# Kernel optimization log

Hardware: AMD Instinct MI355X
Metric: run time of the kernel (lower is better)

## Reference

```python
import jax, jax.numpy as jnp
import numpy as np

DIM = 256
HEADS = 8
H = 56
W = 56
WS = 7          # window size
SHIFT = 3       # cyclic shift
MLP_HIDDEN = 4 * DIM
HEAD_DIM = DIM // HEADS
SCALE = HEAD_DIM ** -0.5
N = WS * WS     # tokens per window
EPS = 1e-5


def _rel_pos_index():
    coords = np.stack(np.meshgrid(np.arange(WS), np.arange(WS), indexing='ij'))  # [2,ws,ws]
    cf = coords.reshape(2, -1)                       # [2, N]
    rel = cf[:, :, None] - cf[:, None, :]            # [2, N, N]
    rel = rel.transpose(1, 2, 0).copy()              # [N, N, 2]
    rel[:, :, 0] += WS - 1
    rel[:, :, 1] += WS - 1
    rel[:, :, 1] *= 2 * WS - 1
    return rel.sum(-1)                               # [N, N]

REL_IDX = jnp.asarray(_rel_pos_index())


def _attn_mask():
    # shifted-window attention mask, computed once (static)
    img = np.zeros((H, W))
    cnt = 0
    slices = (slice(0, -WS), slice(-WS, -SHIFT), slice(-SHIFT, None))
    for hs in slices:
        for ws in slices:
            img[hs, ws] = cnt
            cnt += 1
    mw = img.reshape(H // WS, WS, W // WS, WS).transpose(0, 2, 1, 3).reshape(-1, N)  # [nW, N]
    am = mw[:, None, :] - mw[:, :, None]
    return jnp.asarray(np.where(am != 0, -100.0, 0.0).astype(np.float32))  # [nW, N, N]

ATTN_MASK = _attn_mask()


def _layernorm(y, g, b):
    mu = y.mean(-1, keepdims=True)
    var = ((y - mu) ** 2).mean(-1, keepdims=True)
    return (y - mu) * jax.lax.rsqrt(var + EPS) * g + b


def setup_inputs() -> dict:
    key = jax.random.key(0)
    ks = jax.random.split(key, 10)
    B = 32
    x = jax.random.normal(ks[0], (B, H * W, DIM), dtype=jnp.float32)
    qkv_w = jax.random.normal(ks[1], (DIM, 3 * DIM), dtype=jnp.float32) * 0.02
    qkv_b = jnp.zeros((3 * DIM,), dtype=jnp.float32)
    proj_w = jax.random.normal(ks[2], (DIM, DIM), dtype=jnp.float32) * 0.02
    proj_b = jnp.zeros((DIM,), dtype=jnp.float32)
    bias_table = jax.random.normal(ks[3], ((2 * WS - 1) * (2 * WS - 1), HEADS), dtype=jnp.float32) * 0.02
    norm1_g = jnp.ones((DIM,), dtype=jnp.float32)
    norm1_b = jnp.zeros((DIM,), dtype=jnp.float32)
    norm2_g = jnp.ones((DIM,), dtype=jnp.float32)
    norm2_b = jnp.zeros((DIM,), dtype=jnp.float32)
    mlp_w1 = jax.random.normal(ks[4], (DIM, MLP_HIDDEN), dtype=jnp.float32) * 0.02
    mlp_b1 = jnp.zeros((MLP_HIDDEN,), dtype=jnp.float32)
    mlp_w2 = jax.random.normal(ks[5], (MLP_HIDDEN, DIM), dtype=jnp.float32) * 0.02
    mlp_b2 = jnp.zeros((DIM,), dtype=jnp.float32)
    return dict(x=x, norm1_g=norm1_g, norm1_b=norm1_b, qkv_w=qkv_w, qkv_b=qkv_b,
                proj_w=proj_w, proj_b=proj_b, bias_table=bias_table,
                norm2_g=norm2_g, norm2_b=norm2_b,
                mlp_w1=mlp_w1, mlp_b1=mlp_b1, mlp_w2=mlp_w2, mlp_b2=mlp_b2)


def reference(x, norm1_g, norm1_b, qkv_w, qkv_b, proj_w, proj_b, bias_table,
              norm2_g, norm2_b, mlp_w1, mlp_b1, mlp_w2, mlp_b2):
    B, M, C = x.shape
    shortcut = x
    y = _layernorm(x, norm1_g, norm1_b).reshape(B, H, W, C)
    # cyclic shift
    y = jnp.roll(y, (-SHIFT, -SHIFT), axis=(1, 2))
    # window partition: [B,H,W,C] -> [B*nW, N, C]
    win = y.reshape(B, H // WS, WS, W // WS, WS, C).transpose(0, 1, 3, 2, 4, 5).reshape(-1, N, C)
    Bw = win.shape[0]
    qkv = (win @ qkv_w + qkv_b).reshape(Bw, N, 3, HEADS, HEAD_DIM).transpose(2, 0, 3, 1, 4)
    q, k, v = qkv[0], qkv[1], qkv[2]               # each [Bw, heads, N, hd]
    attn = jnp.einsum('bhnd,bhmd->bhnm', q, k) * SCALE
    bias = bias_table[REL_IDX].transpose(2, 0, 1)  # [heads, N, N]
    attn = attn + bias[None]
    nW = ATTN_MASK.shape[0]
    attn = attn.reshape(B, nW, HEADS, N, N) + ATTN_MASK[None, :, None]
    attn = jax.nn.softmax(attn.reshape(Bw, HEADS, N, N), axis=-1)
    out = jnp.einsum('bhnm,bhmd->bhnd', attn, v).transpose(0, 2, 1, 3).reshape(Bw, N, C)
    out = out @ proj_w + proj_b
    # window reverse and un-shift
    out = out.reshape(B, H // WS, W // WS, WS, WS, C).transpose(0, 1, 3, 2, 4, 5).reshape(B, H, W, C)
    out = jnp.roll(out, (SHIFT, SHIFT), axis=(1, 2)).reshape(B, M, C)
    x = shortcut + out
    h = _layernorm(x, norm2_g, norm2_b)
    h = jax.nn.gelu(h @ mlp_w1 + mlp_b1) @ mlp_w2 + mlp_b2
    return x + h
```

## Files before the change

### kernel.cpp

```cpp
#include <hip/hip_runtime.h>
#include <hip/hip_bf16.h>
#include <math.h>

typedef __bf16 bf16_t;
typedef __attribute__((ext_vector_type(8))) __bf16 bf16x8;
typedef __attribute__((ext_vector_type(4))) __bf16 bf16x4;
typedef __attribute__((ext_vector_type(4))) float f32x4;

#define T_TOK 100352
#define DIMC 256
#define HEADS 8
#define HD 32
#define NTOK 49
#define SHIFT3 3
#define HH 56
#define SCALE_QK 0.17677669529663687f

__device__ __forceinline__ int xrow_of(int rr) {
    int wi = rr / 49; int t = rr - wi * 49;
    int b = wi >> 6; int w64 = wi & 63;
    int wh = w64 >> 3, ww = w64 & 7;
    int i = t / 7, j = t - i * 7;
    int hy = wh * 7 + i, wy = ww * 7 + j;
    int hx = hy + SHIFT3; if (hx >= HH) hx -= HH;
    int wx = wy + SHIFT3; if (wx >= HH) wx -= HH;
    return b * (HH * HH) + hx * HH + wx;
}

__global__ __launch_bounds__(256) void transpose_cast(const float* __restrict__ W,
                                                      bf16_t* __restrict__ WT,
                                                      int K, int Nc) {
    int t = blockIdx.x * 256 + threadIdx.x;
    int k = t / Nc, c = t - k * Nc;
    WT[(size_t)c * K + k] = (bf16_t)W[t];
}

template <int MAP>
__global__ __launch_bounds__(256) void ln_kernel(const float* __restrict__ x,
                                                 const float* __restrict__ g,
                                                 const float* __restrict__ bsh,
                                                 bf16_t* __restrict__ out) {
    int wv = threadIdx.x >> 6, l = threadIdx.x & 63;
    int r = blockIdx.x * 4 + wv;
    int xr = MAP ? xrow_of(r) : r;
    float4 v = ((const float4*)(x + (size_t)xr * DIMC))[l];
    float s = v.x + v.y + v.z + v.w;
    float sq = v.x * v.x + v.y * v.y + v.z * v.z + v.w * v.w;
    #pragma unroll
    for (int off = 32; off; off >>= 1) {
        s += __shfl_down(s, off);
        sq += __shfl_down(sq, off);
    }
    s = __shfl(s, 0); sq = __shfl(sq, 0);
    float mean = s * (1.f / 256.f);
    float var = sq * (1.f / 256.f) - mean * mean;
    float rstd = rsqrtf(var + 1e-5f);
    float4 gv = ((const float4*)g)[l];
    float4 bv = ((const float4*)bsh)[l];
    bf16x4 o;
    o[0] = (bf16_t)((v.x - mean) * rstd * gv.x + bv.x);
    o[1] = (bf16_t)((v.y - mean) * rstd * gv.y + bv.y);
    o[2] = (bf16_t)((v.z - mean) * rstd * gv.z + bv.z);
    o[3] = (bf16_t)((v.w - mean) * rstd * gv.w + bv.w);
    *(bf16x4*)(out + (size_t)r * DIMC + l * 4) = o;
}

template <int EPI, int KT>
__global__ __launch_bounds__(256) void gemm128(const bf16_t* __restrict__ A,
                                               const bf16_t* __restrict__ BT,
                                               const float* __restrict__ bias,
                                               int Nc,
                                               bf16_t* __restrict__ outb,
                                               float* __restrict__ outf,
                                               const float* __restrict__ resid) {
    constexpr int NS = KT / 64;
    __shared__ bf16_t As[2][128 * 64];
    __shared__ bf16_t Bs[2][128 * 64];
    int tid = threadIdx.x;
    int wv = tid >> 6, l = tid & 63;
    int wr = wv >> 1, wc = wv & 1;
    int nTilesN = Nc >> 7;
    int qn = gridDim.x >> 3;
    int lb = (blockIdx.x & 7) * qn + (blockIdx.x >> 3);
    int bm = lb / nTilesN, bn = lb - bm * nTilesN;
    size_t row0 = (size_t)bm * 128;
    int col0 = bn * 128;

    const char* Abase = (const char*)(A + row0 * KT);
    const char* Bbase = (const char*)(BT + (size_t)col0 * KT);
    const size_t ldb = (size_t)KT * 2;

    auto STAGE = [&](int buf, int kk) {
        #pragma unroll
        for (int it = 0; it < 4; ++it) {
            int ci = tid + it * 256;
            int row = ci >> 3, ch = ci & 7;
            int sc = ch ^ (row & 7);
            __builtin_amdgcn_global_load_lds(
                (const __attribute__((address_space(1))) void*)(Abase + (size_t)row * ldb + (size_t)kk * 2 + sc * 16),
                (__attribute__((address_space(3))) void*)((char*)As[buf] + ci * 16), 16, 0, 0);
            __builtin_amdgcn_global_load_lds(
                (const __attribute__((address_space(1))) void*)(Bbase + (size_t)row * ldb + (size_t)kk * 2 + sc * 16),
                (__attribute__((address_space(3))) void*)((char*)Bs[buf] + ci * 16), 16, 0, 0);
        }
    };

    f32x4 acc[4][4] = {};
    const int lr = l & 15, g4 = l >> 4;

    STAGE(0, 0);
    if (NS > 1) STAGE(1, 64);

    #pragma unroll
    for (int s = 0; s < NS; ++s) {
        if (s + 1 < NS) { asm volatile("s_waitcnt vmcnt(8)" ::: "memory"); }
        else            { asm volatile("s_waitcnt vmcnt(0)" ::: "memory"); }
        __builtin_amdgcn_s_barrier();
        __builtin_amdgcn_sched_barrier(0);
        int buf = s & 1;
        #pragma unroll
        for (int ks = 0; ks < 2; ++ks) {
            bf16x8 a[4], b[4];
            #pragma unroll
            for (int mt = 0; mt < 4; ++mt) {
                int rr = wr * 64 + mt * 16 + lr;
                int c = (ks * 4 + g4) ^ (rr & 7);
                a[mt] = *(const bf16x8*)((char*)As[buf] + rr * 128 + c * 16);
            }
            #pragma unroll
            for (int nt = 0; nt < 4; ++nt) {
                int rc = wc * 64 + nt * 16 + lr;
                int c = (ks * 4 + g4) ^ (rc & 7);
                b[nt] = *(const bf16x8*)((char*)Bs[buf] + rc * 128 + c * 16);
            }
            __builtin_amdgcn_s_setprio(1);
            #pragma unroll
            for (int mt = 0; mt < 4; ++mt)
                #pragma unroll
                for (int nt = 0; nt < 4; ++nt)
                    acc[mt][nt] = __builtin_amdgcn_mfma_f32_16x16x32_bf16(a[mt], b[nt], acc[mt][nt], 0, 0, 0);
            __builtin_amdgcn_s_setprio(0);
        }
        __builtin_amdgcn_s_barrier();
        __builtin_amdgcn_sched_barrier(0);
        if (s + 2 < NS) STAGE(buf, (s + 2) * 64);
    }

    #pragma unroll
    for (int m = 0; m < 4; ++m) {
        #pragma unroll
        for (int i = 0; i < 4; ++i) {
            int rr = (int)row0 + wr * 64 + m * 16 + g4 * 4 + i;
            size_t orow = (EPI == 3) ? (size_t)xrow_of(rr) * DIMC : (size_t)rr * Nc;
            #pragma unroll
            for (int n = 0; n < 4; ++n) {
                int cc = col0 + wc * 64 + n * 16 + lr;
                float v = acc[m][n][i] + bias[cc];
                if (EPI == 0) {
                    outb[(size_t)rr * Nc + cc] = (bf16_t)v;
                } else if (EPI == 1) {
                    float t3 = v + 0.044715f * v * v * v;
                    float e = __expf(-1.5957691216057308f * t3);
                    float gl = v * __builtin_amdgcn_rcpf(1.f + e);
                    outb[(size_t)rr * Nc + cc] = (bf16_t)gl;
                } else if (EPI == 2) {
                    size_t o = (size_t)rr * Nc + cc;
                    outf[o] = v + resid[o];
                } else {
                    size_t o = orow + cc;
                    outf[o] = v + resid[o];
                }
            }
        }
    }
}

__global__ __launch_bounds__(256) void attn_mfma(const bf16_t* __restrict__ qkv,
                                                 const float* __restrict__ bt,
                                                 bf16_t* __restrict__ out) {
    __shared__ __align__(16) char lds[4][12800];
    int wv = threadIdx.x >> 6, l = threadIdx.x & 63;
    int head = ((blockIdx.x & 1) << 2) | wv;
    int wi = blockIdx.x >> 1;
    char* W = lds[wv];
    bf16_t* Vt = (bf16_t*)(W + 8192);
    size_t rowbase = (size_t)wi * NTOK;
    const bf16_t* src = qkv + rowbase * 768 + head * HD;

    int w64 = wi & 63;
    int wh = w64 >> 3, ww = w64 & 7;
    bool lastH = (wh == 7), lastW = (ww == 7);
    bool masked = lastH || lastW;

    #pragma unroll
    for (int it = 0; it < 4; ++it) {
        int t = l + it * 64;
        int r = t >> 2, g = t & 3;
        if (r < NTOK) {
            bf16x8 qv = *(const bf16x8*)(src + (size_t)r * 768 + g * 8);
            bf16x8 kv = *(const bf16x8*)(src + (size_t)r * 768 + 256 + g * 8);
            int sa = (r * 64 + g * 16) ^ ((r & 7) << 4);
            *(bf16x8*)(W + sa) = qv;
            *(bf16x8*)(W + 4096 + sa) = kv;
        }
    }
    #pragma unroll
    for (int it = 0; it < 4; ++it) {
        int t = l + it * 64;
        int m = t >> 2, dc = t & 3;
        if (m < NTOK) {
            bf16x8 vv = *(const bf16x8*)(src + (size_t)m * 768 + 512 + dc * 8);
            #pragma unroll
            for (int j = 0; j < 8; ++j) Vt[(dc * 8 + j) * 72 + m] = vv[j];
        } else {
            #pragma unroll
            for (int j = 0; j < 8; ++j) Vt[(dc * 8 + j) * 72 + m] = (bf16_t)0.f;
        }
    }

    int lr = l & 15, g4 = l >> 4;

    bf16x8 a[4], b[4];
    #pragma unroll
    for (int mt = 0; mt < 4; ++mt) {
        int r = mt * 16 + lr;
        int sa = (r * 64 + g4 * 16) ^ ((r & 7) << 4);
        a[mt] = *(const bf16x8*)(W + sa);
        b[mt] = *(const bf16x8*)(W + 4096 + sa);
    }
    f32x4 z = {0.f, 0.f, 0.f, 0.f};
    f32x4 S[4][4];
    #pragma unroll
    for (int mt = 0; mt < 4; ++mt)
        #pragma unroll
        for (int nt = 0; nt < 4; ++nt)
            S[mt][nt] = __builtin_amdgcn_mfma_f32_16x16x32_bf16(a[mt], b[nt], z, 0, 0, 0);

    int i2[4], j2[4], reg2[4];
    #pragma unroll
    for (int nt = 0; nt < 4; ++nt) {
        int cm = nt * 16 + lr;
        i2[nt] = (cm * 147) >> 10;
        j2[nt] = cm - i2[nt] * 7;
        int rh = lastH ? ((i2[nt] < 4) ? 1 : 2) : 0;
        int rw = lastW ? ((j2[nt] < 4) ? 1 : 2) : 0;
        reg2[nt] = rh * 3 + rw;
    }

    #pragma unroll
    for (int mt = 0; mt < 4; ++mt) {
        #pragma unroll
        for (int i = 0; i < 4; ++i) {
            int rn = mt * 16 + g4 * 4 + i;
            bool rowok = rn < NTOK;
            int i1 = (rn * 147) >> 10, j1 = rn - i1 * 7;
            int rh1 = lastH ? ((i1 < 4) ? 1 : 2) : 0;
            int rw1 = lastW ? ((j1 < 4) ? 1 : 2) : 0;
            int reg1 = rh1 * 3 + rw1;
            float sv[4];
            #pragma unroll
            for (int nt = 0; nt < 4; ++nt) {
                int cm = nt * 16 + lr;
                float sc;
                if (rowok && cm < NTOK) {
                    sc = S[mt][nt][i] * SCALE_QK;
                    sc += bt[((i1 - i2[nt] + 6) + 13 * (j1 - j2[nt] + 6)) * 8 + head];
                    if (masked && (reg1 != reg2[nt])) sc -= 100.f;
                } else {
                    sc = -1e30f;
                }
                sv[nt] = sc;
            }
            float mx = fmaxf(fmaxf(sv[0], sv[1]), fmaxf(sv[2], sv[3]));
            mx = fmaxf(mx, __shfl_xor(mx, 1));
            mx = fmaxf(mx, __shfl_xor(mx, 2));
            mx = fmaxf(mx, __shfl_xor(mx, 4));
            mx = fmaxf(mx, __shfl_xor(mx, 8));
            float e[4];
            float sum = 0.f;
            #pragma unroll
            for (int nt = 0; nt < 4; ++nt) { e[nt] = __expf(sv[nt] - mx); sum += e[nt]; }
            sum += __shfl_xor(sum, 1);
            sum += __shfl_xor(sum, 2);
            sum += __shfl_xor(sum, 4);
            sum += __shfl_xor(sum, 8);
            float inv = 1.f / sum;
            #pragma unroll
            for (int nt = 0; nt < 4; ++nt) {
                int cm = nt * 16 + lr;
                int pa = (rn * 128 + cm * 2) ^ ((rn & 7) << 4);
                *(bf16_t*)(W + pa) = (bf16_t)(e[nt] * inv);
            }
        }
    }

    f32x4 o[4][2] = {};
    #pragma unroll
    for (int ks = 0; ks < 2; ++ks) {
        bf16x8 pa[4], vb[2];
        #pragma unroll
        for (int mt = 0; mt < 4; ++mt) {
            int r = mt * 16 + lr;
            int ad = (r * 128 + ks * 64 + g4 * 16) ^ ((r & 7) << 4);
            pa[mt] = *(const bf16x8*)(W + ad);
        }
        #pragma unroll
        for (int dt = 0; dt < 2; ++dt) {
            int d = dt * 16 + lr;
            vb[dt] = *(const bf16x8*)((char*)Vt + d * 144 + ks * 64 + g4 * 16);
        }
        #pragma unroll
        for (int mt = 0; mt < 4; ++mt)
            #pragma unroll
            for (int dt = 0; dt < 2; ++dt)
                o[mt][dt] = __builtin_amdgcn_mfma_f32_16x16x32_bf16(pa[mt], vb[dt], o[mt][dt], 0, 0, 0);
    }

    #pragma unroll
    for (int mt = 0; mt < 4; ++mt) {
        #pragma unroll
        for (int i = 0; i < 4; ++i) {
            int n = mt * 16 + g4 * 4 + i;
            if (n < NTOK) {
                #pragma unroll
                for (int dt = 0; dt < 2; ++dt) {
                    out[(rowbase + n) * DIMC + head * HD + dt * 16 + lr] = (bf16_t)o[mt][dt][i];
                }
            }
        }
    }
}

extern "C" void kernel_launch(void* const* d_in, const int* in_sizes, int n_in,
                              void* d_out, int out_size, void* d_ws, size_t ws_size,
                              hipStream_t stream) {
    const float* x      = (const float*)d_in[0];
    const float* n1g    = (const float*)d_in[1];
    const float* n1b    = (const float*)d_in[2];
    const float* qkv_w  = (const float*)d_in[3];
    const float* qkv_b  = (const float*)d_in[4];
    const float* proj_w = (const float*)d_in[5];
    const float* proj_b = (const float*)d_in[6];
    const float* btab   = (const float*)d_in[7];
    const float* n2g    = (const float*)d_in[8];
    const float* n2b    = (const float*)d_in[9];
    const float* w1     = (const float*)d_in[10];
    const float* b1     = (const float*)d_in[11];
    const float* w2     = (const float*)d_in[12];
    const float* b2     = (const float*)d_in[13];

    char* ws = (char*)d_ws;
    bf16_t* win      = (bf16_t*)(ws);
    bf16_t* qkvbuf   = (bf16_t*)(ws + (size_t)T_TOK * 256 * 2);
    bf16_t* mlp1_buf = (bf16_t*)(ws);
    bf16_t* h2       = (bf16_t*)(ws + (size_t)T_TOK * 2048);
    char* wtp        = ws + (size_t)T_TOK * 2048 + (size_t)T_TOK * 512;
    bf16_t* wt_qkv   = (bf16_t*)wtp;
    bf16_t* wt_proj  = wt_qkv + 768 * 256;
    bf16_t* wt_mlp1  = wt_proj + 256 * 256;
    bf16_t* wt_mlp2  = wt_mlp1 + 1024 * 256;
    float* xmid      = (float*)d_out;

    transpose_cast<<<768, 256, 0, stream>>>(qkv_w, wt_qkv, 256, 768);
    transpose_cast<<<256, 256, 0, stream>>>(proj_w, wt_proj, 256, 256);
    transpose_cast<<<1024, 256, 0, stream>>>(w1, wt_mlp1, 256, 1024);
    transpose_cast<<<1024, 256, 0, stream>>>(w2, wt_mlp2, 1024, 256);

    ln_kernel<1><<<T_TOK / 4, 256, 0, stream>>>(x, n1g, n1b, win);
    gemm128<0, 256><<<(T_TOK / 128) * (768 / 128), 256, 0, stream>>>(win, wt_qkv, qkv_b, 768,
                                                                     qkvbuf, nullptr, nullptr);
    attn_mfma<<<2048 * 2, 256, 0, stream>>>(qkvbuf, btab, win);
    gemm128<3, 256><<<(T_TOK / 128) * (256 / 128), 256, 0, stream>>>(win, wt_proj, proj_b, 256,
                                                                     nullptr, xmid, x);
    ln_kernel<0><<<T_TOK / 4, 256, 0, stream>>>(xmid, n2g, n2b, h2);
    gemm128<1, 256><<<(T_TOK / 128) * (1024 / 128), 256, 0, stream>>>(h2, wt_mlp1, b1, 1024,
                                                                      mlp1_buf, nullptr, nullptr);
    gemm128<2, 1024><<<(T_TOK / 128) * (256 / 128), 256, 0, stream>>>(mlp1_buf, wt_mlp2, b2, 256,
                                                                      nullptr, xmid, xmid);
}
```

Measured before the change: 547.0 us.

## Fuse projection GEMM with residual and LayerNorm2; shrink GEMM K-tile to 32

Adds a proj_ln kernel that computes the attention output projection over 64-row by 256-column tiles. In the same kernel it adds bias and the residual, scatters rows back to the unshifted token order, and applies LayerNorm2. It writes both xmid and the bf16 normalized h2, which removes the separate LayerNorm launch and its extra pass over the fp32 activations. Separately, the generic gemm128 K-step drops from 64 to 32 with a one-stage-ahead prefetch and 4-chunk swizzle. That lowers LDS use but doubles the barriers per K.

After: 617.3 us. 12.8% more time.

```diff
diff --git a/kernel.cpp b/kernel.cpp
--- a/kernel.cpp
+++ b/kernel.cpp
@@ -35,14 +35,13 @@
     WT[(size_t)c * K + k] = (bf16_t)W[t];
 }
 
-template <int MAP>
 __global__ __launch_bounds__(256) void ln_kernel(const float* __restrict__ x,
                                                  const float* __restrict__ g,
                                                  const float* __restrict__ bsh,
                                                  bf16_t* __restrict__ out) {
     int wv = threadIdx.x >> 6, l = threadIdx.x & 63;
     int r = blockIdx.x * 4 + wv;
-    int xr = MAP ? xrow_of(r) : r;
+    int xr = xrow_of(r);
     float4 v = ((const float4*)(x + (size_t)xr * DIMC))[l];
     float s = v.x + v.y + v.z + v.w;
     float sq = v.x * v.x + v.y * v.y + v.z * v.z + v.w * v.w;
@@ -73,9 +72,9 @@
                                                bf16_t* __restrict__ outb,
                                                float* __restrict__ outf,
                                                const float* __restrict__ resid) {
-    constexpr int NS = KT / 64;
-    __shared__ bf16_t As[2][128 * 64];
-    __shared__ bf16_t Bs[2][128 * 64];
+    constexpr int NS = KT / 32;
+    __shared__ bf16_t As[2][128 * 32];
+    __shared__ bf16_t Bs[2][128 * 32];
     int tid = threadIdx.x;
     int wv = tid >> 6, l = tid & 63;
     int wr = wv >> 1, wc = wv & 1;
@@ -92,10 +91,10 @@
 
     auto STAGE = [&](int buf, int kk) {
         #pragma unroll
-        for (int it = 0; it < 4; ++it) {
+        for (int it = 0; it < 2; ++it) {
             int ci = tid + it * 256;
-            int row = ci >> 3, ch = ci & 7;
-            int sc = ch ^ (row & 7);
+            int row = ci >> 2, ch = ci & 3;
+            int sc = ch ^ (row & 3);
             __builtin_amdgcn_global_load_lds(
                 (const __attribute__((address_space(1))) void*)(Abase + (size_t)row * ldb + (size_t)kk * 2 + sc * 16),
                 (__attribute__((address_space(3))) void*)((char*)As[buf] + ci * 16), 16, 0, 0);
@@ -109,41 +108,39 @@
     const int lr = l & 15, g4 = l >> 4;
 
     STAGE(0, 0);
-    if (NS > 1) STAGE(1, 64);
-
-    #pragma unroll
+
     for (int s = 0; s < NS; ++s) {
-        if (s + 1 < NS) { asm volatile("s_waitcnt vmcnt(8)" ::: "memory"); }
-        else            { asm volatile("s_waitcnt vmcnt(0)" ::: "memory"); }
+        int buf = s & 1;
+        if (s + 1 < NS) {
+            STAGE(buf ^ 1, (s + 1) * 32);
+            asm volatile("s_waitcnt vmcnt(4)" ::: "memory");
+        } else {
+            asm volatile("s_waitcnt vmcnt(0)" ::: "memory");
+        }
         __builtin_amdgcn_s_barrier();
         __builtin_amdgcn_sched_barrier(0);
-        int buf = s & 1;
-        #pragma unroll
-        for (int ks = 0; ks < 2; ++ks) {
-            bf16x8 a[4], b[4];
-            #pragma unroll
-            for (int mt = 0; mt < 4; ++mt) {
-                int rr = wr * 64 + mt * 16 + lr;
-                int c = (ks * 4 + g4) ^ (rr & 7);
-                a[mt] = *(const bf16x8*)((char*)As[buf] + rr * 128 + c * 16);
-            }
-            #pragma unroll
-            for (int nt = 0; nt < 4; ++nt) {
-                int rc = wc * 64 + nt * 16 + lr;
-                int c = (ks * 4 + g4) ^ (rc & 7);
-                b[nt] = *(const bf16x8*)((char*)Bs[buf] + rc * 128 + c * 16);
-            }
-            __builtin_amdgcn_s_setprio(1);
-            #pragma unroll
-            for (int mt = 0; mt < 4; ++mt)
-                #pragma unroll
-                for (int nt = 0; nt < 4; ++nt)
-                    acc[mt][nt] = __builtin_amdgcn_mfma_f32_16x16x32_bf16(a[mt], b[nt], acc[mt][nt], 0, 0, 0);
-            __builtin_amdgcn_s_setprio(0);
-        }
+        bf16x8 a[4], b[4];
+        #pragma unroll
+        for (int mt = 0; mt < 4; ++mt) {
+            int rr = wr * 64 + mt * 16 + lr;
+            int c = g4 ^ (rr & 3);
+            a[mt] = *(const bf16x8*)((char*)As[buf] + rr * 64 + c * 16);
+        }
+        #pragma unroll
+        for (int nt = 0; nt < 4; ++nt) {
+            int rc = wc * 64 + nt * 16 + lr;
+            int c = g4 ^ (rc & 3);
+            b[nt] = *(const bf16x8*)((char*)Bs[buf] + rc * 64 + c * 16);
+        }
+        __builtin_amdgcn_s_setprio(1);
+        #pragma unroll
+        for (int mt = 0; mt < 4; ++mt)
+            #pragma unroll
+            for (int nt = 0; nt < 4; ++nt)
+                acc[mt][nt] = __builtin_amdgcn_mfma_f32_16x16x32_bf16(a[mt], b[nt], acc[mt][nt], 0, 0, 0);
+        __builtin_amdgcn_s_setprio(0);
+        __builtin_amdgcn_sched_barrier(0);
         __builtin_amdgcn_s_barrier();
-        __builtin_amdgcn_sched_barrier(0);
-        if (s + 2 < NS) STAGE(buf, (s + 2) * 64);
     }
 
     #pragma unroll
@@ -151,7 +148,6 @@
         #pragma unroll
         for (int i = 0; i < 4; ++i) {
             int rr = (int)row0 + wr * 64 + m * 16 + g4 * 4 + i;
-            size_t orow = (EPI == 3) ? (size_t)xrow_of(rr) * DIMC : (size_t)rr * Nc;
             #pragma unroll
             for (int n = 0; n < 4; ++n) {
                 int cc = col0 + wc * 64 + n * 16 + lr;
@@ -163,14 +159,128 @@
                     float e = __expf(-1.5957691216057308f * t3);
                     float gl = v * __builtin_amdgcn_rcpf(1.f + e);
                     outb[(size_t)rr * Nc + cc] = (bf16_t)gl;
-                } else if (EPI == 2) {
+                } else {
                     size_t o = (size_t)rr * Nc + cc;
-                    outf[o] = v + resid[o];
-                } else {
-                    size_t o = orow + cc;
                     outf[o] = v + resid[o];
                 }
             }
+        }
+    }
+}
+
+__global__ __launch_bounds__(256) void proj_ln(const bf16_t* __restrict__ A,
+                                               const bf16_t* __restrict__ BT,
+                                               const float* __restrict__ bias,
+                                               const float* __restrict__ x,
+                                               const float* __restrict__ g2,
+                                               const float* __restrict__ b2,
+                                               float* __restrict__ xmid,
+                                               bf16_t* __restrict__ h2) {
+    constexpr int NS = 8;
+    __shared__ bf16_t As[2][64 * 32];
+    __shared__ bf16_t Bs[2][256 * 32];
+    int tid = threadIdx.x;
+    int wv = tid >> 6, l = tid & 63;
+    int lr = l & 15, g4 = l >> 4;
+    int qn = gridDim.x >> 3;
+    int lb = (blockIdx.x & 7) * qn + (blockIdx.x >> 3);
+    size_t row0 = (size_t)lb * 64;
+
+    const char* Abase = (const char*)(A + row0 * 256);
+    const char* Bbase = (const char*)BT;
+
+    auto STAGE = [&](int buf, int kk) {
+        {
+            int ci = tid;
+            int row = ci >> 2, ch = ci & 3;
+            int sc = ch ^ (row & 3);
+            __builtin_amdgcn_global_load_lds(
+                (const __attribute__((address_space(1))) void*)(Abase + (size_t)row * 512 + (size_t)kk * 2 + sc * 16),
+                (__attribute__((address_space(3))) void*)((char*)As[buf] + ci * 16), 16, 0, 0);
+        }
+        #pragma unroll
+        for (int it = 0; it < 4; ++it) {
+            int ci = tid + it * 256;
+            int row = ci >> 2, ch = ci & 3;
+            int sc = ch ^ (row & 3);
+            __builtin_amdgcn_global_load_lds(
+                (const __attribute__((address_space(1))) void*)(Bbase + (size_t)row * 512 + (size_t)kk * 2 + sc * 16),
+                (__attribute__((address_space(3))) void*)((char*)Bs[buf] + ci * 16), 16, 0, 0);
+        }
+    };
+
+    f32x4 acc[16] = {};
+
+    STAGE(0, 0);
+
+    for (int s = 0; s < NS; ++s) {
+        int buf = s & 1;
+        if (s + 1 < NS) {
+            STAGE(buf ^ 1, (s + 1) * 32);
+            asm volatile("s_waitcnt vmcnt(5)" ::: "memory");
+        } else {
+            asm volatile("s_waitcnt vmcnt(0)" ::: "memory");
+        }
+        __builtin_amdgcn_s_barrier();
+        __builtin_amdgcn_sched_barrier(0);
+        bf16x8 a;
+        {
+            int rr = wv * 16 + lr;
+            int c = g4 ^ (rr & 3);
+            a = *(const bf16x8*)((char*)As[buf] + rr * 64 + c * 16);
+        }
+        bf16x8 b[16];
+        #pragma unroll
+        for (int nt = 0; nt < 16; ++nt) {
+            int rc = nt * 16 + lr;
+            int c = g4 ^ (rc & 3);
+            b[nt] = *(const bf16x8*)((char*)Bs[buf] + rc * 64 + c * 16);
+        }
+        __builtin_amdgcn_s_setprio(1);
+        #pragma unroll
+        for (int nt = 0; nt < 16; ++nt)
+            acc[nt] = __builtin_amdgcn_mfma_f32_16x16x32_bf16(a, b[nt], acc[nt], 0, 0, 0);
+        __builtin_amdgcn_s_setprio(0);
+        __builtin_amdgcn_sched_barrier(0);
+        __builtin_amdgcn_s_barrier();
+    }
+
+    int xr[4];
+    #pragma unroll
+    for (int i = 0; i < 4; ++i) xr[i] = xrow_of((int)row0 + wv * 16 + g4 * 4 + i);
+
+    float psum[4] = {0.f, 0.f, 0.f, 0.f}, psq[4] = {0.f, 0.f, 0.f, 0.f};
+    #pragma unroll
+    for (int n = 0; n < 16; ++n) {
+        int cc = n * 16 + lr;
+        float bv = bias[cc];
+        #pragma unroll
+        for (int i = 0; i < 4; ++i) {
+            float v = acc[n][i] + bv + x[(size_t)xr[i] * 256 + cc];
+            psum[i] += v; psq[i] += v * v;
+        }
+    }
+    float mean[4], rstd[4];
+    #pragma unroll
+    for (int i = 0; i < 4; ++i) {
+        float s = psum[i], q = psq[i];
+        s += __shfl_xor(s, 1); q += __shfl_xor(q, 1);
+        s += __shfl_xor(s, 2); q += __shfl_xor(q, 2);
+        s += __shfl_xor(s, 4); q += __shfl_xor(q, 4);
+        s += __shfl_xor(s, 8); q += __shfl_xor(q, 8);
+        mean[i] = s * (1.f / 256.f);
+        rstd[i] = rsqrtf(q * (1.f / 256.f) - mean[i] * mean[i] + 1e-5f);
+    }
+    #pragma unroll
+    for (int n = 0; n < 16; ++n) {
+        int cc = n * 16 + lr;
+        float bv = bias[cc], gv = g2[cc], b2v = b2[cc];
+        #pragma unroll
+        for (int i = 0; i < 4; ++i) {
+            size_t o = (size_t)xr[i] * 256 + cc;
+            float v = acc[n][i] + bv + x[o];
+            xmid[o] = v;
+            h2[o] = (bf16_t)((v - mean[i]) * rstd[i] * gv + b2v);
         }
     }
 }
@@ -366,13 +476,11 @@
     transpose_cast<<<1024, 256, 0, stream>>>(w1, wt_mlp1, 256, 1024);
     transpose_cast<<<1024, 256, 0, stream>>>(w2, wt_mlp2, 1024, 256);
 
-    ln_kernel<1><<<T_TOK / 4, 256, 0, stream>>>(x, n1g, n1b, win);
+    ln_kernel<<<T_TOK / 4, 256, 0, stream>>>(x, n1g, n1b, win);
     gemm128<0, 256><<<(T_TOK / 128) * (768 / 128), 256, 0, stream>>>(win, wt_qkv, qkv_b, 768,
                                                                      qkvbuf, nullptr, nullptr);
     attn_mfma<<<2048 * 2, 256, 0, stream>>>(qkvbuf, btab, win);
-    gemm128<3, 256><<<(T_TOK / 128) * (256 / 128), 256, 0, stream>>>(win, wt_proj, proj_b, 256,
-                                                                     nullptr, xmid, x);
-    ln_kernel<0><<<T_TOK / 4, 256, 0, stream>>>(xmid, n2g, n2b, h2);
+    proj_ln<<<T_TOK / 64, 256, 0, stream>>>(win, wt_proj, proj_b, x, n2g, n2b, xmid, h2);
     gemm128<1, 256><<<(T_TOK / 128) * (1024 / 128), 256, 0, stream>>>(h2, wt_mlp1, b1, 1024,
                                                                       mlp1_buf, nullptr, nullptr);
     gemm128<2, 1024><<<(T_TOK / 128) * (256 / 128), 256, 0, stream>>>(mlp1_buf, wt_mlp2, b2, 256,
```

## Use triple-buffered K=32 stages with interleaved A/B LDS tile in gemm128

Applied to the files above, without the earlier changes.

The GEMM mainloop moves from double-buffered K=64 stages to triple-buffered K=32 stages. Each stage packs the A and B rows into one 16KB LDS tile with an XOR swizzle across 8 chunks. The next-next stage is issued right after the barrier and before compute, which removes the second barrier per iteration and shrinks LDS from 64KB to 48KB, possibly allowing higher occupancy. The trade-off is twice as many barrier iterations with fewer MFMAs between syncs, and correctness of reusing a buffer without a trailing barrier depends on the 3-deep ring.

Result: faster. 535.7 us (-2.1%).

```diff
diff --git a/kernel.cpp b/kernel.cpp
--- a/kernel.cpp
+++ b/kernel.cpp
@@ -73,9 +73,8 @@
                                                bf16_t* __restrict__ outb,
                                                float* __restrict__ outf,
                                                const float* __restrict__ resid) {
-    constexpr int NS = KT / 64;
-    __shared__ bf16_t As[2][128 * 64];
-    __shared__ bf16_t Bs[2][128 * 64];
+    constexpr int NS = KT / 32;
+    __shared__ __align__(16) char S[3][16384];
     int tid = threadIdx.x;
     int wv = tid >> 6, l = tid & 63;
     int wr = wv >> 1, wc = wv & 1;
@@ -90,18 +89,18 @@
     const char* Bbase = (const char*)(BT + (size_t)col0 * KT);
     const size_t ldb = (size_t)KT * 2;
 
-    auto STAGE = [&](int buf, int kk) {
+    auto STAGE = [&](int b, int kk) {
         #pragma unroll
         for (int it = 0; it < 4; ++it) {
             int ci = tid + it * 256;
-            int row = ci >> 3, ch = ci & 7;
-            int sc = ch ^ (row & 7);
+            int row = ci >> 3, p = ci & 7;
+            int up = p ^ (row & 7);
+            const char* gsrc = (up < 4)
+                ? (Abase + (size_t)row * ldb + (size_t)kk * 2 + up * 16)
+                : (Bbase + (size_t)row * ldb + (size_t)kk * 2 + (up - 4) * 16);
             __builtin_amdgcn_global_load_lds(
-                (const __attribute__((address_space(1))) void*)(Abase + (size_t)row * ldb + (size_t)kk * 2 + sc * 16),
-                (__attribute__((address_space(3))) void*)((char*)As[buf] + ci * 16), 16, 0, 0);
-            __builtin_amdgcn_global_load_lds(
-                (const __attribute__((address_space(1))) void*)(Bbase + (size_t)row * ldb + (size_t)kk * 2 + sc * 16),
-                (__attribute__((address_space(3))) void*)((char*)Bs[buf] + ci * 16), 16, 0, 0);
+                (const __attribute__((address_space(1))) void*)gsrc,
+                (__attribute__((address_space(3))) void*)(S[b] + ci * 16), 16, 0, 0);
         }
     };
 
@@ -109,41 +108,38 @@
     const int lr = l & 15, g4 = l >> 4;
 
     STAGE(0, 0);
-    if (NS > 1) STAGE(1, 64);
+    STAGE(1, 32);
 
     #pragma unroll
     for (int s = 0; s < NS; ++s) {
-        if (s + 1 < NS) { asm volatile("s_waitcnt vmcnt(8)" ::: "memory"); }
+        if (s + 1 < NS) { asm volatile("s_waitcnt vmcnt(4)" ::: "memory"); }
         else            { asm volatile("s_waitcnt vmcnt(0)" ::: "memory"); }
         __builtin_amdgcn_s_barrier();
         __builtin_amdgcn_sched_barrier(0);
-        int buf = s & 1;
-        #pragma unroll
-        for (int ks = 0; ks < 2; ++ks) {
-            bf16x8 a[4], b[4];
-            #pragma unroll
-            for (int mt = 0; mt < 4; ++mt) {
-                int rr = wr * 64 + mt * 16 + lr;
-                int c = (ks * 4 + g4) ^ (rr & 7);
-                a[mt] = *(const bf16x8*)((char*)As[buf] + rr * 128 + c * 16);
-            }
-            #pragma unroll
-            for (int nt = 0; nt < 4; ++nt) {
-                int rc = wc * 64 + nt * 16 + lr;
-                int c = (ks * 4 + g4) ^ (rc & 7);
-                b[nt] = *(const bf16x8*)((char*)Bs[buf] + rc * 128 + c * 16);
-            }
-            __builtin_amdgcn_s_setprio(1);
-            #pragma unroll
-            for (int mt = 0; mt < 4; ++mt)
-                #pragma unroll
-                for (int nt = 0; nt < 4; ++nt)
-                    acc[mt][nt] = __builtin_amdgcn_mfma_f32_16x16x32_bf16(a[mt], b[nt], acc[mt][nt], 0, 0, 0);
-            __builtin_amdgcn_s_setprio(0);
-        }
-        __builtin_amdgcn_s_barrier();
+        int buf = s % 3;
+        if (s + 2 < NS) STAGE((s + 2) % 3, (s + 2) * 32);
+        const char* Sb = S[buf];
+        bf16x8 a[4], b[4];
+        #pragma unroll
+        for (int mt = 0; mt < 4; ++mt) {
+            int rr = wr * 64 + mt * 16 + lr;
+            int p = g4 ^ (rr & 7);
+            a[mt] = *(const bf16x8*)(Sb + rr * 128 + p * 16);
+        }
+        #pragma unroll
+        for (int nt = 0; nt < 4; ++nt) {
+            int rc = wc * 64 + nt * 16 + lr;
+            int p = (4 + g4) ^ (rc & 7);
+            b[nt] = *(const bf16x8*)(Sb + rc * 128 + p * 16);
+        }
+        __builtin_amdgcn_s_setprio(1);
+        #pragma unroll
+        for (int mt = 0; mt < 4; ++mt)
+            #pragma unroll
+            for (int nt = 0; nt < 4; ++nt)
+                acc[mt][nt] = __builtin_amdgcn_mfma_f32_16x16x32_bf16(a[mt], b[nt], acc[mt][nt], 0, 0, 0);
+        __builtin_amdgcn_s_setprio(0);
         __builtin_amdgcn_sched_barrier(0);
-        if (s + 2 < NS) STAGE(buf, (s + 2) * 64);
     }
 
     #pragma unroll
```
